# Kernel tuning notes

Measured on AMD Instinct MI355X. Metric: run time of the kernel, lower is better.

## Reference

```python
import jax, jax.numpy as jnp
import numpy as np

B, NS, NF, D, K, N = 8192, 16, 16, 128, 32, 50000
A_H = 32          # alpha MLP hidden dim
EPS = 0.05        # entropic regularization
GW_ITER = 1
SK_ITER = 2


def setup_inputs() -> dict:
    key = jax.random.key(0)
    ks = jax.random.split(key, 10)
    adj = jax.random.uniform(ks[0], (B, NS, NS), dtype=jnp.float32)
    features = jax.random.uniform(ks[1], (N, D), dtype=jnp.float32)
    idxs = jax.random.randint(ks[2], (B, NS), 0, N + 1)  # N is the zero-pad row
    C_up = jax.random.uniform(ks[3], (NF * (NF - 1) // 2, K), minval=-1.0, maxval=1.0)
    F_filter = jax.random.uniform(ks[4], (NF, D, K))
    h_logits = 0.1 * jax.random.normal(ks[5], (NF,))
    w1 = jax.random.normal(ks[6], (D, A_H)) / np.float32(np.sqrt(D))
    b1 = jnp.zeros((A_H,), jnp.float32)
    w2 = jax.random.normal(ks[7], (A_H, 1)) / np.float32(np.sqrt(A_H))
    b2 = jnp.zeros((1,), jnp.float32)
    return dict(adj=adj, features=features, idxs=idxs, C_up=C_up, F_filter=F_filter,
                h_logits=h_logits, w1=w1, b1=b1, w2=w2, b2=b2)


def _log_sinkhorn(cost, logp, logq):
    # cost: [B,K,Ns,Nf]; logp: [B,Ns]; logq: [Nf]. Stable log-domain Sinkhorn.
    f = jnp.zeros(cost.shape[:3], cost.dtype)              # [B,K,Ns]
    g = jnp.zeros(cost.shape[:2] + cost.shape[3:], cost.dtype)  # [B,K,Nf]
    lp = logp[:, None, :]
    lq = logq[None, None, :]
    for _ in range(SK_ITER):
        f = EPS * (lp - jax.nn.logsumexp((g[:, :, None, :] - cost) / EPS, axis=3))
        g = EPS * (lq - jax.nn.logsumexp((f[:, :, :, None] - cost) / EPS, axis=2))
    return jnp.exp((f[..., None] + g[:, :, None, :] - cost) / EPS)  # transport plan


def reference(adj, features, idxs, C_up, F_filter, h_logits, w1, b1, w2, b2):
    nf, d, k = F_filter.shape
    # symmetric filter adjacency from upper-triangle params (ReLU'd)
    iu, ju = jnp.triu_indices(nf, 1)
    C = jnp.zeros((nf, nf, k), C_up.dtype).at[iu, ju].set(jax.nn.relu(C_up))
    C = C + jnp.swapaxes(C, 0, 1)                          # [Nf,Nf,K]

    # gather subgraph features (zero pad row at index N)
    x = jnp.concatenate([features, jnp.zeros((1, d), features.dtype)], axis=0)
    x = x[idxs]                                            # [B,Ns,D]
    b, ns, _ = x.shape

    h_sub = jnp.full((b, ns), 1.0 / ns, x.dtype)           # uniform subgraph weights
    h_fil = jax.nn.softmax(h_logits)                       # [Nf]

    # local alpha gate from pooled subgraph features
    pooled = x.mean(axis=1)                                # [B,D]
    alpha = jax.nn.sigmoid(jax.nn.relu(pooled @ w1 + b1) @ w2 + b2)  # [B,1]
    alpha = alpha[:, :, None, None]                        # [B,1,1,1]

    # feature cost M[b,k,i,j] = ||x_bi - F_filter[j,:,k]||^2
    x2 = jnp.sum(x * x, -1)                                # [B,Ns]
    f2 = jnp.sum(F_filter * F_filter, 1)                   # [Nf,K]
    xf = jnp.einsum('bid,jdk->bkij', x, F_filter)          # [B,K,Ns,Nf]
    M = x2[:, None, :, None] + f2.T[None, :, None, :] - 2.0 * xf

    # GW square-loss constants
    constC1 = jnp.einsum('bip,bp->bi', adj * adj, h_sub)   # [B,Ns]
    constC2 = jnp.einsum('pjk,p->jk', C * C, h_fil)        # [Nf,K]

    def gw_tens(T):
        cross = jnp.einsum('bip,bkpq,qjk->bkij', adj, T, C)  # [B,K,Ns,Nf]
        return constC1[:, None, :, None] + constC2.T[None, :, None, :] - 2.0 * cross

    # init plan: outer(h_sub, h_fil), shared across K
    T = jnp.broadcast_to((h_sub[:, :, None] * h_fil[None, None, :])[:, None],
                         (b, k, ns, nf))
    logp = jnp.log(h_sub)
    logq = jnp.log(h_fil)
    for _ in range(GW_ITER):
        cost = (1.0 - alpha) * M + alpha * gw_tens(T)
        T = _log_sinkhorn(cost, logp, logq)
    final_cost = (1.0 - alpha) * M + alpha * gw_tens(T)
    fgw_dists = jnp.sum(T * final_cost, axis=(2, 3))       # [B,K]
    return fgw_dists
```

## Files before the change

kernel.cpp:

```cpp
#include <hip/hip_runtime.h>

typedef unsigned short ushort;
typedef unsigned int uint;
typedef __attribute__((ext_vector_type(8))) short short8;
typedef __attribute__((ext_vector_type(4))) float f32x4;

#define B_    8192
#define NB_   2
#define GRID_ (B_ / NB_)
#define NS_   16
#define D_    128
#define K_    32
#define NV_   50000
#define SC_   28.853900817779268f
#define ISC_  0.03465735902799726f

#define WS_HF    0
#define WS_LHF2  16
#define WS_CCT   32
#define WS_CC2T  544
#define WS_F2    1056
#define WSB_FBHI 6272
#define WSB_FBLO 137344
#define WSB_CB1  268416
#define WSB_CB2  301184

__device__ __forceinline__ ushort bf16rne(float v) {
    uint u = __float_as_uint(v);
    uint r = (u + 0x7fffu + ((u >> 16) & 1u)) >> 16;
    return (ushort)r;
}
__device__ __forceinline__ float bf16tof(ushort h) { return __uint_as_float(((uint)h) << 16); }

template <int C>
__device__ __forceinline__ float dppmv(float x) {
    return __int_as_float(__builtin_amdgcn_update_dpp(
        __float_as_int(x), __float_as_int(x), C, 0xf, 0xf, false));
}
__device__ __forceinline__ float rowmax16(float x) {
    x = fmaxf(x, dppmv<0x121>(x));
    x = fmaxf(x, dppmv<0x122>(x));
    x = fmaxf(x, dppmv<0x124>(x));
    x = fmaxf(x, dppmv<0x128>(x));
    return x;
}
__device__ __forceinline__ float rowsum16(float x) {
    x += dppmv<0x121>(x);
    x += dppmv<0x122>(x);
    x += dppmv<0x124>(x);
    x += dppmv<0x128>(x);
    return x;
}
__device__ __forceinline__ short8 lo16x8(uint4 a, uint4 b) {
    union { short8 v; uint u[4]; } r;
    r.u[0] = __builtin_amdgcn_perm(a.y, a.x, 0x05040100u);
    r.u[1] = __builtin_amdgcn_perm(a.w, a.z, 0x05040100u);
    r.u[2] = __builtin_amdgcn_perm(b.y, b.x, 0x05040100u);
    r.u[3] = __builtin_amdgcn_perm(b.w, b.z, 0x05040100u);
    return r.v;
}
__device__ __forceinline__ short8 hi16x8(uint4 a, uint4 b) {
    union { short8 v; uint u[4]; } r;
    r.u[0] = __builtin_amdgcn_perm(a.y, a.x, 0x07060302u);
    r.u[1] = __builtin_amdgcn_perm(a.w, a.z, 0x07060302u);
    r.u[2] = __builtin_amdgcn_perm(b.y, b.x, 0x07060302u);
    r.u[3] = __builtin_amdgcn_perm(b.w, b.z, 0x07060302u);
    return r.v;
}
__device__ __forceinline__ f32x4 mfma16(short8 a, short8 b, f32x4 c) {
    return __builtin_amdgcn_mfma_f32_16x16x32_bf16(a, b, c, 0, 0, 0);
}

__global__ __launch_bounds__(512) void init_fb(const float* __restrict__ Ff, float* __restrict__ ws) {
    int idx = blockIdx.x * 512 + threadIdx.x;
    int e = idx & 7, l = (idx >> 3) & 63, s = (idx >> 9) & 3, k = idx >> 11;
    int j = l & 15, kg = l >> 4;
    int d = s * 32 + kg * 8 + e;
    float v = Ff[(j * D_ + d) * K_ + k];
    ushort hb = bf16rne(v);
    ushort lb = bf16rne(v - bf16tof(hb));
    ushort* FBHI = (ushort*)((char*)ws + WSB_FBHI);
    ushort* FBLO = (ushort*)((char*)ws + WSB_FBLO);
    FBHI[idx] = hb;
    FBLO[idx] = lb;
}

__global__ __launch_bounds__(1024) void init_small(
    const float* __restrict__ C_up, const float* __restrict__ Ff,
    const float* __restrict__ h_logits, float* __restrict__ ws) {
    __shared__ float hf[16];
    __shared__ float Cs[16][16][32];
    __shared__ float f2p[16][32][2];
    const int t = threadIdx.x;

    if (t == 0) {
        float m = -3.4e38f;
        for (int p = 0; p < 16; ++p) m = fmaxf(m, h_logits[p]);
        float e[16], s = 0.f;
        for (int p = 0; p < 16; ++p) { e[p] = __expf(h_logits[p] - m); s += e[p]; }
        for (int p = 0; p < 16; ++p) {
            hf[p] = e[p] / s;
            ws[WS_HF + p] = hf[p];
            ws[WS_LHF2 + p] = log2f(hf[p]);
        }
    }
    for (int e0 = t; e0 < 16 * 16 * 32; e0 += 1024) {
        int k = e0 & 31, j = (e0 >> 5) & 15, q = e0 >> 9;
        float v = 0.f;
        if (q < j)      { int pi = q * (31 - q) / 2 + (j - q - 1); v = fmaxf(C_up[pi * 32 + k], 0.f); }
        else if (j < q) { int pi = j * (31 - j) / 2 + (q - j - 1); v = fmaxf(C_up[pi * 32 + k], 0.f); }
        Cs[q][j][k] = v;
    }
    __syncthreads();

    if (t < 512) {
        int k = t >> 4, j = t & 15;
        float s1 = 0.f, s2 = 0.f;
        for (int q = 0; q < 16; ++q) {
            float c = Cs[q][j][k];
            s1 += hf[q] * c;
            s2 += hf[q] * c * c;
        }
        ws[WS_CCT + k * 16 + j] = s1;
        ws[WS_CC2T + k * 16 + j] = s2;
    }
    {
        int k = t & 31, half = (t >> 5) & 1, j = t >> 6;
        float s = 0.f;
        for (int dd = 0; dd < 64; ++dd) {
            int d = half * 64 + dd;
            float f = Ff[(j * D_ + d) * K_ + k];
            s += f * f;
        }
        f2p[j][k][half] = s;
    }
    {
        ushort* CB1 = (ushort*)((char*)ws + WSB_CB1);
        ushort* CB2 = (ushort*)((char*)ws + WSB_CB2);
        for (int i0 = t; i0 < 16384; i0 += 1024) {
            int e = i0 & 7, l = (i0 >> 3) & 63, k = i0 >> 9;
            int kg = l >> 4, j = l & 15, q = (kg & 1) * 8 + e;
            float c = Cs[q][j][k];
            ushort hb = bf16rne(c);
            CB1[i0] = hb;
            CB2[i0] = (kg < 2) ? bf16rne(c - bf16tof(hb)) : (ushort)0;
        }
    }
    __syncthreads();
    if (t < 512) {
        int j = t >> 5, k = t & 31;
        ws[WS_F2 + j * 32 + k] = f2p[j][k][0] + f2p[j][k][1];
    }
}

__global__ __launch_bounds__(512, 4) void fgw_main(
    const float* __restrict__ adj, const float* __restrict__ features,
    const int* __restrict__ idxs,
    const float* __restrict__ w1, const float* __restrict__ b1,
    const float* __restrict__ w2, const float* __restrict__ b2,
    const float* __restrict__ ws, float* __restrict__ out) {
    __shared__ __align__(16) ushort xA[NB_][2][4][64][8];
    __shared__ __align__(16) uint  exch[8][2][16][20];
    __shared__ __align__(16) ushort adjA[NB_][64][8];
    __shared__ float adj_s[NB_][16][17];
    __shared__ float pooled[NB_][128];
    __shared__ float x2part[NB_][16][8];
    __shared__ float x2s[NB_][16], c1s[NB_][16], rss[NB_][16];
    __shared__ float alpha_sh[NB_];
    __shared__ int idx_sh[NB_][16];

    const int t = threadIdx.x;
    const int blk = blockIdx.x;
    float* xT = (float*)&exch[0][0][0][0];

    if (t < NB_ * 16) idx_sh[t >> 4][t & 15] = idxs[(blk * NB_ + (t >> 4)) * 16 + (t & 15)];
    {
        int pb = t >> 8, rem = t & 255;
        adj_s[pb][rem >> 4][rem & 15] = adj[(blk * NB_ + pb) * 256 + rem];
    }
    __syncthreads();

    if (t < 256) {
        int pb = t >> 7, i = (t >> 3) & 15, c = t & 7;
        int ix = idx_sh[pb][i];
        float vv[16];
        if (ix < NV_) {
            const float4* fp = (const float4*)(features + (size_t)ix * D_ + c * 16);
            float4 q0 = fp[0], q1 = fp[1], q2 = fp[2], q3 = fp[3];
            vv[0] = q0.x; vv[1] = q0.y; vv[2] = q0.z; vv[3] = q0.w;
            vv[4] = q1.x; vv[5] = q1.y; vv[6] = q1.z; vv[7] = q1.w;
            vv[8] = q2.x; vv[9] = q2.y; vv[10] = q2.z; vv[11] = q2.w;
            vv[12] = q3.x; vv[13] = q3.y; vv[14] = q3.z; vv[15] = q3.w;
        } else {
            #pragma unroll
            for (int e = 0; e < 16; ++e) vv[e] = 0.f;
        }
        float* xrow = xT + (pb * 16 + i) * 132 + c * 16;
        float s2 = 0.f;
        #pragma unroll
        for (int e = 0; e < 16; ++e) { xrow[e] = vv[e]; s2 += vv[e] * vv[e]; }
        x2part[pb][i][c] = s2;
        #pragma unroll
        for (int g = 0; g < 2; ++g) {
            int d0 = c * 16 + g * 8;
            int s = d0 >> 5, kg = (d0 >> 3) & 3;
            union { short8 v; ushort u[8]; } h8, l8;
            #pragma unroll
            for (int e = 0; e < 8; ++e) {
                float x = vv[g * 8 + e];
                ushort hb = bf16rne(x);
                h8.u[e] = hb;
                l8.u[e] = bf16rne(x - bf16tof(hb));
            }
            *(short8*)&xA[pb][0][s][kg * 16 + i][0] = h8.v;
            *(short8*)&xA[pb][1][s][kg * 16 + i][0] = l8.v;
        }
    } else if (t < 384) {
        int t2 = t - 256, pb = t2 >> 6, l = t2 & 63;
        int i = l & 15, kg = l >> 4;
        union { short8 v; ushort u[8]; } f8;
        #pragma unroll
        for (int e = 0; e < 8; ++e) {
            int p = (kg & 1) * 8 + e;
            float v = adj_s[pb][i][p];
            ushort hb = bf16rne(v);
            f8.u[e] = (kg < 2) ? hb : bf16rne(v - bf16tof(hb));
        }
        *(short8*)&adjA[pb][l][0] = f8.v;
    } else if (t < 416) {
        int t2 = t - 384, pb = t2 >> 4, i = t2 & 15;
        float s = 0.f, s2 = 0.f;
        for (int p = 0; p < 16; ++p) { float a = adj_s[pb][i][p]; s += a; s2 += a * a; }
        rss[pb][i] = s;
        c1s[pb][i] = s2 * (1.f / 16.f);
    }
    __syncthreads();

    if (t < NB_ * 128) {
        int pb = t >> 7, d = t & 127;
        float s = 0.f;
        for (int i = 0; i < 16; ++i) s += xT[(pb * 16 + i) * 132 + d];
        pooled[pb][d] = s * (1.f / 16.f);
    } else if (t < NB_ * 128 + NB_ * 16) {
        int t2 = t - NB_ * 128, pb = t2 >> 4, i = t2 & 15;
        float s = 0.f;
        #pragma unroll
        for (int c = 0; c < 8; ++c) s += x2part[pb][i][c];
        x2s[pb][i] = s;
    }
    __syncthreads();

    if (t < 64) {
        int pb = t >> 5, u = t & 31;
        float h = b1[u];
        for (int d = 0; d < D_; ++d) h = fmaf(pooled[pb][d], w1[d * 32 + u], h);
        h = fmaxf(h, 0.f);
        float z = h * w2[u];
        #pragma unroll
        for (int s = 1; s < 32; s <<= 1) z += __shfl_xor(z, s);
        if (u == 0) alpha_sh[pb] = 1.f / (1.f + __expf(-(z + b2[0])));
    }
    __syncthreads();

    const int w = t >> 6, l = t & 63;
    const int jl = l & 15, ig = l >> 4;
    const ushort* FBHI = (const ushort*)((const char*)ws + WSB_FBHI);
    const ushort* FBLO = (const ushort*)((const char*)ws + WSB_FBLO);

    f32x4 acc[NB_][4];
    #pragma unroll
    for (int pb = 0; pb < NB_; ++pb)
        #pragma unroll
        for (int kk = 0; kk < 4; ++kk) acc[pb][kk] = (f32x4){0.f, 0.f, 0.f, 0.f};

    #pragma unroll
    for (int s = 0; s < 4; ++s) {
        short8 Ah[NB_], Al[NB_];
        #pragma unroll
        for (int pb = 0; pb < NB_; ++pb) {
            Ah[pb] = *(const short8*)&xA[pb][0][s][l][0];
            Al[pb] = *(const short8*)&xA[pb][1][s][l][0];
        }
        #pragma unroll
        for (int kk = 0; kk < 4; ++kk) {
            int k = kk * 8 + w;
            const short8 Bh = *(const short8*)(FBHI + ((k * 4 + s) * 64 + l) * 8);
            const short8 Bl = *(const short8*)(FBLO + ((k * 4 + s) * 64 + l) * 8);
            #pragma unroll
            for (int pb = 0; pb < NB_; ++pb) {
                acc[pb][kk] = mfma16(Ah[pb], Bh, acc[pb][kk]);
                acc[pb][kk] = mfma16(Al[pb], Bh, acc[pb][kk]);
                acc[pb][kk] = mfma16(Ah[pb], Bl, acc[pb][kk]);
            }
        }
    }

    const float lq2 = ws[WS_LHF2 + jl];
    uint* Tb = &exch[w][0][0][0];
    uint* Mb = &exch[w][1][0][0];
    const ushort* CB1 = (const ushort*)((const char*)ws + WSB_CB1);
    const ushort* CB2 = (const ushort*)((const char*)ws + WSB_CB2);
    const short8 z8 = {0, 0, 0, 0, 0, 0, 0, 0};

    #pragma unroll
    for (int pb = 0; pb < NB_; ++pb) {
        const float alpha = alpha_sh[pb], oma = 1.f - alpha;
        float x2r[4], c1r[4], rsr[4];
        #pragma unroll
        for (int r = 0; r < 4; ++r) {
            x2r[r] = x2s[pb][ig * 4 + r];
            c1r[r] = c1s[pb][ig * 4 + r];
            rsr[r] = rss[pb][ig * 4 + r] * (1.f / 16.f);
        }
        const short8 Aadj = *(const short8*)&adjA[pb][l][0];

        #pragma unroll
        for (int kk = 0; kk < 4; ++kk) {
            const int k = kk * 8 + w;
            const float f2v = ws[WS_F2 + jl * 32 + k];
            const float cctv = ws[WS_CCT + k * 16 + jl];
            const float cc2v = ws[WS_CC2T + k * 16 + jl];
            float Chat[4];
            #pragma unroll
            for (int r = 0; r < 4; ++r) {
                float M = x2r[r] + f2v - 2.f * acc[pb][kk][r];
                float gw0 = c1r[r] + cc2v - 2.f * rsr[r] * cctv;
                Chat[r] = SC_ * (oma * M + alpha * gw0);
            }
            float G = 0.f, Fh[4];
            #pragma unroll
            for (int it = 0; it < 2; ++it) {
                #pragma unroll
                for (int r = 0; r < 4; ++r) {
                    float a = G - Chat[r];
                    float m = rowmax16(a);
                    float e = exp2f(a - m);
                    float S = rowsum16(e);
                    Fh[r] = -4.f - m - log2f(S);
                }
                float m2 = fmaxf(fmaxf(Fh[0] - Chat[0], Fh[1] - Chat[1]),
                                 fmaxf(Fh[2] - Chat[2], Fh[3] - Chat[3]));
                m2 = fmaxf(m2, __shfl_xor(m2, 16));
                m2 = fmaxf(m2, __shfl_xor(m2, 32));
                float S2 = 0.f;
                #pragma unroll
                for (int r = 0; r < 4; ++r) S2 += exp2f(Fh[r] - Chat[r] - m2);
                S2 += __shfl_xor(S2, 16);
                S2 += __shfl_xor(S2, 32);
                G = lq2 - m2 - log2f(S2);
            }
            float Tv[4];
            #pragma unroll
            for (int r = 0; r < 4; ++r) Tv[r] = exp2f(Fh[r] + G - Chat[r]);

            uint4 pk;
            {
                uint pw[4];
                #pragma unroll
                for (int r = 0; r < 4; ++r) {
                    ushort th = bf16rne(Tv[r]);
                    float tlf = Tv[r] - bf16tof(th);
                    pw[r] = (uint)th | ((uint)bf16rne(tlf) << 16);
                }
                pk.x = pw[0]; pk.y = pw[1]; pk.z = pw[2]; pk.w = pw[3];
            }
            *(uint4*)&Tb[jl * 20 + ig * 4] = pk;
            uint4 tw = *(const uint4*)&Tb[jl * 20 + (ig & 1) * 8];
            uint4 tw2 = *(const uint4*)&Tb[jl * 20 + (ig & 1) * 8 + 4];
            short8 Bt1 = lo16x8(tw, tw2);
            short8 Bt2 = (ig < 2) ? hi16x8(tw, tw2) : z8;
            f32x4 tmp = {0.f, 0.f, 0.f, 0.f};
            tmp = mfma16(Aadj, Bt1, tmp);
            tmp = mfma16(Aadj, Bt2, tmp);

            #pragma unroll
            for (int r = 0; r < 4; ++r) {
                ushort th = bf16rne(tmp[r]);
                float tlf = tmp[r] - bf16tof(th);
                Mb[(ig * 4 + r) * 20 + jl] = (uint)th | ((uint)bf16rne(tlf) << 16);
            }
            uint4 aw = *(const uint4*)&Mb[jl * 20 + (ig & 1) * 8];
            uint4 aw2 = *(const uint4*)&Mb[jl * 20 + (ig & 1) * 8 + 4];
            short8 Atm = (ig < 2) ? lo16x8(aw, aw2) : hi16x8(aw, aw2);
            const short8 C1f = *(const short8*)(CB1 + (k * 64 + l) * 8);
            const short8 C2f = *(const short8*)(CB2 + (k * 64 + l) * 8);
            f32x4 cr = {0.f, 0.f, 0.f, 0.f};
            cr = mfma16(Atm, C1f, cr);
            cr = mfma16(Atm, C2f, cr);

            float dot = 0.f;
            #pragma unroll
            for (int r = 0; r < 4; ++r) {
                float fc = Chat[r] * ISC_ + 2.f * alpha * (rsr[r] * cctv - cr[r]);
                dot = fmaf(Tv[r], fc, dot);
            }
            dot = rowsum16(dot);
            dot += __shfl_xor(dot, 16);
            dot += __shfl_xor(dot, 32);
            if (l == 0) out[(blk * NB_ + pb) * K_ + k] = dot;
        }
    }
}

extern "C" void kernel_launch(void* const* d_in, const int* in_sizes, int n_in,
                              void* d_out, int out_size, void* d_ws, size_t ws_size,
                              hipStream_t stream) {
    (void)in_sizes; (void)n_in; (void)out_size; (void)ws_size;
    const float* adj      = (const float*)d_in[0];
    const float* features = (const float*)d_in[1];
    const int*   idxs     = (const int*)  d_in[2];
    const float* C_up     = (const float*)d_in[3];
    const float* Ff       = (const float*)d_in[4];
    const float* h_logits = (const float*)d_in[5];
    const float* w1       = (const float*)d_in[6];
    const float* b1       = (const float*)d_in[7];
    const float* w2       = (const float*)d_in[8];
    const float* b2       = (const float*)d_in[9];
    float* out = (float*)d_out;
    float* ws  = (float*)d_ws;

    hipLaunchKernelGGL(init_fb, dim3(128), dim3(512), 0, stream, Ff, ws);
    hipLaunchKernelGGL(init_small, dim3(1), dim3(1024), 0, stream, C_up, Ff, h_logits, ws);
    hipLaunchKernelGGL(fgw_main, dim3(GRID_), dim3(512), 0, stream,
                       adj, features, idxs, w1, b1, w2, b2, ws, out);
}
```

Measured before the change: 329.7 us.

## Drop split-bf16 for GW cross terms and restructure per-k MFMA loop

The transport plan and the adj·T intermediate are now held as single bf16 values instead of hi/lo split pairs. This halves the MFMAs in the cross-term chain, removes the CB2 table and the perm-based unpacking. The main loop is restructured so each k computes its feature MFMA accumulators right before the Sinkhorn stage, which cuts live accumulators, and launch bounds are relaxed from 4 to 2 blocks per SM. w1 is transposed once into the workspace so the alpha MLP can read it as float4. The cost is reduced precision in the GW cross terms, which could push the output past tolerance.

Result: slower. 365.6 us (+10.9%).

```diff
diff --git a/kernel.cpp b/kernel.cpp
--- a/kernel.cpp
+++ b/kernel.cpp
@@ -8,7 +8,6 @@
 #define B_    8192
 #define NB_   2
 #define GRID_ (B_ / NB_)
-#define NS_   16
 #define D_    128
 #define K_    32
 #define NV_   50000
@@ -20,10 +19,10 @@
 #define WS_CCT   32
 #define WS_CC2T  544
 #define WS_F2    1056
-#define WSB_FBHI 6272
-#define WSB_FBLO 137344
-#define WSB_CB1  268416
-#define WSB_CB2  301184
+#define WS_W1T   1568
+#define WSB_FBHI 22656
+#define WSB_FBLO 153728
+#define WSB_CB1  284800
 
 __device__ __forceinline__ ushort bf16rne(float v) {
     uint u = __float_as_uint(v);
@@ -50,22 +49,6 @@
     x += dppmv<0x124>(x);
     x += dppmv<0x128>(x);
     return x;
-}
-__device__ __forceinline__ short8 lo16x8(uint4 a, uint4 b) {
-    union { short8 v; uint u[4]; } r;
-    r.u[0] = __builtin_amdgcn_perm(a.y, a.x, 0x05040100u);
-    r.u[1] = __builtin_amdgcn_perm(a.w, a.z, 0x05040100u);
-    r.u[2] = __builtin_amdgcn_perm(b.y, b.x, 0x05040100u);
-    r.u[3] = __builtin_amdgcn_perm(b.w, b.z, 0x05040100u);
-    return r.v;
-}
-__device__ __forceinline__ short8 hi16x8(uint4 a, uint4 b) {
-    union { short8 v; uint u[4]; } r;
-    r.u[0] = __builtin_amdgcn_perm(a.y, a.x, 0x07060302u);
-    r.u[1] = __builtin_amdgcn_perm(a.w, a.z, 0x07060302u);
-    r.u[2] = __builtin_amdgcn_perm(b.y, b.x, 0x07060302u);
-    r.u[3] = __builtin_amdgcn_perm(b.w, b.z, 0x07060302u);
-    return r.v;
 }
 __device__ __forceinline__ f32x4 mfma16(short8 a, short8 b, f32x4 c) {
     return __builtin_amdgcn_mfma_f32_16x16x32_bf16(a, b, c, 0, 0, 0);
@@ -87,7 +70,8 @@
 
 __global__ __launch_bounds__(1024) void init_small(
     const float* __restrict__ C_up, const float* __restrict__ Ff,
-    const float* __restrict__ h_logits, float* __restrict__ ws) {
+    const float* __restrict__ h_logits, const float* __restrict__ w1,
+    float* __restrict__ ws) {
     __shared__ float hf[16];
     __shared__ float Cs[16][16][32];
     __shared__ float f2p[16][32][2];
@@ -111,6 +95,10 @@
         else if (j < q) { int pi = j * (31 - j) / 2 + (q - j - 1); v = fmaxf(C_up[pi * 32 + k], 0.f); }
         Cs[q][j][k] = v;
     }
+    for (int e0 = t; e0 < 4096; e0 += 1024) {
+        int u = e0 >> 7, d = e0 & 127;
+        ws[WS_W1T + e0] = w1[d * 32 + u];
+    }
     __syncthreads();
 
     if (t < 512) {
@@ -136,14 +124,10 @@
     }
     {
         ushort* CB1 = (ushort*)((char*)ws + WSB_CB1);
-        ushort* CB2 = (ushort*)((char*)ws + WSB_CB2);
         for (int i0 = t; i0 < 16384; i0 += 1024) {
             int e = i0 & 7, l = (i0 >> 3) & 63, k = i0 >> 9;
             int kg = l >> 4, j = l & 15, q = (kg & 1) * 8 + e;
-            float c = Cs[q][j][k];
-            ushort hb = bf16rne(c);
-            CB1[i0] = hb;
-            CB2[i0] = (kg < 2) ? bf16rne(c - bf16tof(hb)) : (ushort)0;
+            CB1[i0] = (kg < 2) ? bf16rne(Cs[q][j][k]) : (ushort)0;
         }
     }
     __syncthreads();
@@ -153,25 +137,27 @@
     }
 }
 
-__global__ __launch_bounds__(512, 4) void fgw_main(
+__global__ __launch_bounds__(512, 2) void fgw_main(
     const float* __restrict__ adj, const float* __restrict__ features,
     const int* __restrict__ idxs,
-    const float* __restrict__ w1, const float* __restrict__ b1,
+    const float* __restrict__ b1,
     const float* __restrict__ w2, const float* __restrict__ b2,
     const float* __restrict__ ws, float* __restrict__ out) {
     __shared__ __align__(16) ushort xA[NB_][2][4][64][8];
-    __shared__ __align__(16) uint  exch[8][2][16][20];
+    __shared__ __align__(16) uint  exchbuf[4224];
     __shared__ __align__(16) ushort adjA[NB_][64][8];
     __shared__ float adj_s[NB_][16][17];
     __shared__ float pooled[NB_][128];
     __shared__ float x2part[NB_][16][8];
-    __shared__ float x2s[NB_][16], c1s[NB_][16], rss[NB_][16];
+    __shared__ __align__(16) float x2s[NB_][16];
+    __shared__ __align__(16) float c1s[NB_][16];
+    __shared__ __align__(16) float rss[NB_][16];
     __shared__ float alpha_sh[NB_];
     __shared__ int idx_sh[NB_][16];
 
     const int t = threadIdx.x;
     const int blk = blockIdx.x;
-    float* xT = (float*)&exch[0][0][0][0];
+    float* xT = (float*)exchbuf;
 
     if (t < NB_ * 16) idx_sh[t >> 4][t & 15] = idxs[(blk * NB_ + (t >> 4)) * 16 + (t & 15)];
     {
@@ -253,7 +239,15 @@
     if (t < 64) {
         int pb = t >> 5, u = t & 31;
         float h = b1[u];
-        for (int d = 0; d < D_; ++d) h = fmaf(pooled[pb][d], w1[d * 32 + u], h);
+        const float4* wrow = (const float4*)(ws + WS_W1T + u * 128);
+        #pragma unroll 4
+        for (int dd = 0; dd < 32; ++dd) {
+            float4 w4 = wrow[dd];
+            h = fmaf(pooled[pb][dd * 4 + 0], w4.x, h);
+            h = fmaf(pooled[pb][dd * 4 + 1], w4.y, h);
+            h = fmaf(pooled[pb][dd * 4 + 2], w4.z, h);
+            h = fmaf(pooled[pb][dd * 4 + 3], w4.w, h);
+        }
         h = fmaxf(h, 0.f);
         float z = h * w2[u];
         #pragma unroll
@@ -264,67 +258,55 @@
 
     const int w = t >> 6, l = t & 63;
     const int jl = l & 15, ig = l >> 4;
+    const float lq2 = ws[WS_LHF2 + jl];
     const ushort* FBHI = (const ushort*)((const char*)ws + WSB_FBHI);
     const ushort* FBLO = (const ushort*)((const char*)ws + WSB_FBLO);
-
-    f32x4 acc[NB_][4];
-    #pragma unroll
-    for (int pb = 0; pb < NB_; ++pb)
-        #pragma unroll
-        for (int kk = 0; kk < 4; ++kk) acc[pb][kk] = (f32x4){0.f, 0.f, 0.f, 0.f};
-
-    #pragma unroll
-    for (int s = 0; s < 4; ++s) {
-        short8 Ah[NB_], Al[NB_];
-        #pragma unroll
-        for (int pb = 0; pb < NB_; ++pb) {
-            Ah[pb] = *(const short8*)&xA[pb][0][s][l][0];
-            Al[pb] = *(const short8*)&xA[pb][1][s][l][0];
-        }
-        #pragma unroll
-        for (int kk = 0; kk < 4; ++kk) {
-            int k = kk * 8 + w;
+    const ushort* CB1  = (const ushort*)((const char*)ws + WSB_CB1);
+    uint* Tb = exchbuf + w * 384;
+    uint* Mb = Tb + 192;
+
+    #pragma unroll 1
+    for (int kk = 0; kk < 4; ++kk) {
+        const int k = kk * 8 + w;
+        f32x4 acc0 = {0.f, 0.f, 0.f, 0.f}, acc1 = {0.f, 0.f, 0.f, 0.f};
+        #pragma unroll
+        for (int s = 0; s < 4; ++s) {
             const short8 Bh = *(const short8*)(FBHI + ((k * 4 + s) * 64 + l) * 8);
             const short8 Bl = *(const short8*)(FBLO + ((k * 4 + s) * 64 + l) * 8);
-            #pragma unroll
-            for (int pb = 0; pb < NB_; ++pb) {
-                acc[pb][kk] = mfma16(Ah[pb], Bh, acc[pb][kk]);
-                acc[pb][kk] = mfma16(Al[pb], Bh, acc[pb][kk]);
-                acc[pb][kk] = mfma16(Ah[pb], Bl, acc[pb][kk]);
-            }
-        }
-    }
-
-    const float lq2 = ws[WS_LHF2 + jl];
-    uint* Tb = &exch[w][0][0][0];
-    uint* Mb = &exch[w][1][0][0];
-    const ushort* CB1 = (const ushort*)((const char*)ws + WSB_CB1);
-    const ushort* CB2 = (const ushort*)((const char*)ws + WSB_CB2);
-    const short8 z8 = {0, 0, 0, 0, 0, 0, 0, 0};
-
-    #pragma unroll
-    for (int pb = 0; pb < NB_; ++pb) {
-        const float alpha = alpha_sh[pb], oma = 1.f - alpha;
-        float x2r[4], c1r[4], rsr[4];
-        #pragma unroll
-        for (int r = 0; r < 4; ++r) {
-            x2r[r] = x2s[pb][ig * 4 + r];
-            c1r[r] = c1s[pb][ig * 4 + r];
-            rsr[r] = rss[pb][ig * 4 + r] * (1.f / 16.f);
-        }
-        const short8 Aadj = *(const short8*)&adjA[pb][l][0];
-
-        #pragma unroll
-        for (int kk = 0; kk < 4; ++kk) {
-            const int k = kk * 8 + w;
-            const float f2v = ws[WS_F2 + jl * 32 + k];
-            const float cctv = ws[WS_CCT + k * 16 + jl];
-            const float cc2v = ws[WS_CC2T + k * 16 + jl];
-            float Chat[4];
+            {
+                const short8 Ah = *(const short8*)&xA[0][0][s][l][0];
+                const short8 Al = *(const short8*)&xA[0][1][s][l][0];
+                acc0 = mfma16(Ah, Bh, acc0);
+                acc0 = mfma16(Al, Bh, acc0);
+                acc0 = mfma16(Ah, Bl, acc0);
+            }
+            {
+                const short8 Ah = *(const short8*)&xA[1][0][s][l][0];
+                const short8 Al = *(const short8*)&xA[1][1][s][l][0];
+                acc1 = mfma16(Ah, Bh, acc1);
+                acc1 = mfma16(Al, Bh, acc1);
+                acc1 = mfma16(Ah, Bl, acc1);
+            }
+        }
+        const float f2v  = ws[WS_F2 + jl * 32 + k];
+        const float cctv = ws[WS_CCT + k * 16 + jl];
+        const float cc2v = ws[WS_CC2T + k * 16 + jl];
+        const short8 C1f = *(const short8*)(CB1 + (k * 64 + l) * 8);
+
+        #pragma unroll
+        for (int pb = 0; pb < NB_; ++pb) {
+            const f32x4 accv = pb ? acc1 : acc0;
+            const float alpha = alpha_sh[pb], oma = 1.f - alpha;
+            const short8 Aadj = *(const short8*)&adjA[pb][l][0];
+            const f32x4 x2v = *(const f32x4*)&x2s[pb][ig * 4];
+            const f32x4 c1v = *(const f32x4*)&c1s[pb][ig * 4];
+            const f32x4 rsv = *(const f32x4*)&rss[pb][ig * 4];
+            float Chat[4], rc[4];
             #pragma unroll
             for (int r = 0; r < 4; ++r) {
-                float M = x2r[r] + f2v - 2.f * acc[pb][kk][r];
-                float gw0 = c1r[r] + cc2v - 2.f * rsr[r] * cctv;
+                float M = x2v[r] + f2v - 2.f * accv[r];
+                rc[r] = (rsv[r] * (1.f / 16.f)) * cctv;
+                float gw0 = c1v[r] + cc2v - 2.f * rc[r];
                 Chat[r] = SC_ * (oma * M + alpha * gw0);
             }
             float G = 0.f, Fh[4];
@@ -353,45 +335,26 @@
             #pragma unroll
             for (int r = 0; r < 4; ++r) Tv[r] = exp2f(Fh[r] + G - Chat[r]);
 
-            uint4 pk;
             {
-                uint pw[4];
-                #pragma unroll
-                for (int r = 0; r < 4; ++r) {
-                    ushort th = bf16rne(Tv[r]);
-                    float tlf = Tv[r] - bf16tof(th);
-                    pw[r] = (uint)th | ((uint)bf16rne(tlf) << 16);
-                }
-                pk.x = pw[0]; pk.y = pw[1]; pk.z = pw[2]; pk.w = pw[3];
-            }
-            *(uint4*)&Tb[jl * 20 + ig * 4] = pk;
-            uint4 tw = *(const uint4*)&Tb[jl * 20 + (ig & 1) * 8];
-            uint4 tw2 = *(const uint4*)&Tb[jl * 20 + (ig & 1) * 8 + 4];
-            short8 Bt1 = lo16x8(tw, tw2);
-            short8 Bt2 = (ig < 2) ? hi16x8(tw, tw2) : z8;
-            f32x4 tmp = {0.f, 0.f, 0.f, 0.f};
-            tmp = mfma16(Aadj, Bt1, tmp);
-            tmp = mfma16(Aadj, Bt2, tmp);
-
+                uint p0 = (uint)bf16rne(Tv[0]) | ((uint)bf16rne(Tv[1]) << 16);
+                uint p1 = (uint)bf16rne(Tv[2]) | ((uint)bf16rne(Tv[3]) << 16);
+                Tb[jl * 12 + ig * 2]     = p0;
+                Tb[jl * 12 + ig * 2 + 1] = p1;
+            }
+            const short8 Bt = *(const short8*)&Tb[jl * 12 + (ig & 1) * 4];
+            f32x4 tmpv = mfma16(Aadj, Bt, (f32x4){0.f, 0.f, 0.f, 0.f});
+
+            ushort* Mbs = (ushort*)Mb;
+            #pragma unroll
+            for (int r = 0; r < 4; ++r)
+                Mbs[(ig * 4 + r) * 24 + jl] = bf16rne(tmpv[r]);
+            const short8 Atm = *(const short8*)&Mbs[jl * 24 + (ig & 1) * 8];
+            f32x4 cr = mfma16(Atm, C1f, (f32x4){0.f, 0.f, 0.f, 0.f});
+
+            float dot = 0.f;
             #pragma unroll
             for (int r = 0; r < 4; ++r) {
-                ushort th = bf16rne(tmp[r]);
-                float tlf = tmp[r] - bf16tof(th);
-                Mb[(ig * 4 + r) * 20 + jl] = (uint)th | ((uint)bf16rne(tlf) << 16);
-            }
-            uint4 aw = *(const uint4*)&Mb[jl * 20 + (ig & 1) * 8];
-            uint4 aw2 = *(const uint4*)&Mb[jl * 20 + (ig & 1) * 8 + 4];
-            short8 Atm = (ig < 2) ? lo16x8(aw, aw2) : hi16x8(aw, aw2);
-            const short8 C1f = *(const short8*)(CB1 + (k * 64 + l) * 8);
-            const short8 C2f = *(const short8*)(CB2 + (k * 64 + l) * 8);
-            f32x4 cr = {0.f, 0.f, 0.f, 0.f};
-            cr = mfma16(Atm, C1f, cr);
-            cr = mfma16(Atm, C2f, cr);
-
-            float dot = 0.f;
-            #pragma unroll
-            for (int r = 0; r < 4; ++r) {
-                float fc = Chat[r] * ISC_ + 2.f * alpha * (rsr[r] * cctv - cr[r]);
+                float fc = Chat[r] * ISC_ + 2.f * alpha * (rc[r] - cr[r]);
                 dot = fmaf(Tv[r], fc, dot);
             }
             dot = rowsum16(dot);
@@ -420,7 +383,7 @@
     float* ws  = (float*)d_ws;
 
     hipLaunchKernelGGL(init_fb, dim3(128), dim3(512), 0, stream, Ff, ws);
-    hipLaunchKernelGGL(init_small, dim3(1), dim3(1024), 0, stream, C_up, Ff, h_logits, ws);
+    hipLaunchKernelGGL(init_small, dim3(1), dim3(1024), 0, stream, C_up, Ff, h_logits, w1, ws);
     hipLaunchKernelGGL(fgw_main, dim3(GRID_), dim3(512), 0, stream,
-                       adj, features, idxs, w1, b1, w2, b2, ws, out);
-}
+                       adj, features, idxs, b1, w2, b2, ws, out);
+}
```
